# Performance work log

Hardware: AMD Instinct MI355X
Metric: run time of the kernel (lower is better)

The kernel has to match this reference:

```python
import jax, jax.numpy as jnp
import numpy as np

NUM_HEADS = 16
THETA = 10000.0


def setup_inputs() -> dict:
    key = jax.random.key(0)
    k1, k2, k3, k4 = jax.random.split(key, 4)
    B, T, D = 2, 2048, 1024
    x = jax.random.normal(k1, (B, T, D), dtype=jnp.float32)
    token_positions = jnp.sort(
        jax.random.randint(k2, (B, T), 0, 2048), axis=-1
    ).astype(jnp.int32)
    sigma_qkv = float(np.sqrt(2.0 / (D + 3 * D)))
    sigma_out = float(np.sqrt(2.0 / (D + D)))
    W_qkv = jax.random.normal(k3, (3 * D, D), dtype=jnp.float32) * sigma_qkv
    W_out = jax.random.normal(k4, (D, D), dtype=jnp.float32) * sigma_out
    return {"x": x, "token_positions": token_positions, "W_qkv": W_qkv, "W_out": W_out}


def _apply_rope(t, cos, sin):
    # t: [B, H, T, d_k]; cos/sin: [B, T, d_k//2]
    B, H, T, dk = t.shape
    t2 = t.reshape(B, H, T, dk // 2, 2)
    te, to = t2[..., 0], t2[..., 1]
    c = cos[:, None]  # [B, 1, T, dk//2]
    s = sin[:, None]
    ye = te * c - to * s
    yo = to * c + te * s
    return jnp.stack([ye, yo], axis=-1).reshape(B, H, T, dk)


def reference(x, token_positions, W_qkv, W_out):
    B, T, D = x.shape
    H = NUM_HEADS
    dk = D // H

    # fused QKV projection: [B, T, 3D] -> split (three, h, d) on last dim
    qkv = jnp.einsum("btd,od->bto", x, W_qkv).reshape(B, T, 3, H, dk)
    qkv = jnp.transpose(qkv, (2, 0, 3, 1, 4))  # [3, B, H, T, dk]
    q, k, v = qkv[0], qkv[1], qkv[2]

    # RoPE angles from token positions
    n = jnp.arange(dk // 2, dtype=jnp.float32)
    inv_freq = THETA ** (-2.0 * n / dk)  # [dk//2]
    angles = token_positions.astype(jnp.float32)[..., None] * inv_freq  # [B, T, dk//2]
    cos, sin = jnp.cos(angles), jnp.sin(angles)
    q = _apply_rope(q, cos, sin)
    k = _apply_rope(k, cos, sin)

    # causal scaled dot-product attention
    scores = jnp.einsum("bhid,bhjd->bhij", q, k) / jnp.sqrt(jnp.float32(dk))
    causal = jnp.tril(jnp.ones((T, T), dtype=bool))
    scores = jnp.where(causal, scores, -jnp.inf)
    probs = jax.nn.softmax(scores, axis=-1)
    attn = jnp.einsum("bhij,bhjd->bhid", probs, v)  # [B, H, T, dk]

    concat = jnp.transpose(attn, (0, 2, 1, 3)).reshape(B, T, D)
    return jnp.einsum("btd,od->bto", concat, W_out)
```

## Files before the change

### kernel.cpp

```cpp
#include <hip/hip_runtime.h>
#include <hip/hip_bf16.h>
#include <cmath>

#define T_SEQ 2048
#define D_MODEL 1024
#define NHEAD 16
#define DK 64

typedef short bf16x8 __attribute__((ext_vector_type(8)));
typedef float f32x4 __attribute__((ext_vector_type(4)));
typedef float f32x16 __attribute__((ext_vector_type(16)));
typedef unsigned uint2v __attribute__((ext_vector_type(2)));

union U8 { unsigned u[4]; bf16x8 v; };

#define VMCNT(n) asm volatile("s_waitcnt vmcnt(" #n ")" ::: "memory")
#define BAR() __builtin_amdgcn_s_barrier()
#define SFENCE() __builtin_amdgcn_sched_barrier(0)

__device__ __forceinline__ short f2b(float f) {
    unsigned u = __builtin_bit_cast(unsigned, f);
    unsigned r = (u + 0x7FFFu + ((u >> 16) & 1u)) >> 16;
    return (short)r;
}

__device__ __forceinline__ void gll16(const void* g, void* l) {
    __builtin_amdgcn_global_load_lds(
        (__attribute__((address_space(1))) void*)g,
        (__attribute__((address_space(3))) void*)l, 16, 0, 0);
}

__device__ __forceinline__ bf16x8 lds_frag(const short* base, int row, int chunk) {
    return *reinterpret_cast<const bf16x8*>(
        (const char*)base + row * 128 + ((chunk * 16) ^ ((row & 7) << 4)));
}

__device__ __forceinline__ unsigned pkbf16(float a, float b) {
    unsigned r;
    asm("v_cvt_pk_bf16_f32 %0, %1, %2" : "=v"(r) : "v"(a), "v"(b));
    return r;
}
__device__ __forceinline__ void pl32swap(unsigned& a, unsigned& b) {
    uint2v r = __builtin_amdgcn_permlane32_swap(a, b, false, false);
    a = r.x; b = r.y;
}

__global__ __launch_bounds__(256) void cvt_all(const float* __restrict__ x,
                                               const float* __restrict__ wq,
                                               const float* __restrict__ wo,
                                               const int* __restrict__ pos,
                                               short* __restrict__ xb,
                                               short* __restrict__ wqb,
                                               short* __restrict__ wob,
                                               float* __restrict__ ct,
                                               float* __restrict__ st) {
    int i = blockIdx.x * 256 + threadIdx.x;
    if (i >= 1048576) {
        int j = i - 1048576;
        int bt = j >> 5, n = j & 31;
        float p = (float)pos[bt];
        float invf = expf((float)n * (-2.0f / (float)DK) * 9.210340371976184f);
        float s, c;
        sincosf(p * invf, &s, &c);
        ct[j] = c; st[j] = s;
        return;
    }
    const float* src;
    short* dst;
    int srcoff, c;
    if (i < 524288) {
        c = i;
        int tile = c >> 9, cc = c & 511;
        int kblk = cc >> 7, row = cc & 127;
        int rb = tile >> 5, kb = tile & 31;
        srcoff = (rb * 128 + row) * D_MODEL + kb * 32 + kblk * 8;
        src = x; dst = xb;
    } else if (i < 917504) {
        c = i - 524288;
        int tile = c >> 9, cc = c & 511;
        int kblk = cc >> 7, row = cc & 127;
        int rb = tile >> 5, kb = tile & 31;
        srcoff = (rb * 128 + row) * D_MODEL + kb * 32 + kblk * 8;
        src = wq; dst = wqb;
    } else {
        c = i - 917504;
        int tile = c >> 8, cc = c & 255;
        int kblk = cc >> 6, row = cc & 63;
        int nb = tile >> 5, kb = tile & 31;
        srcoff = (nb * 64 + row) * D_MODEL + kb * 32 + kblk * 8;
        src = wo; dst = wob;
    }
    float4 a = *reinterpret_cast<const float4*>(src + srcoff);
    float4 b = *reinterpret_cast<const float4*>(src + srcoff + 4);
    bf16x8 v;
    v[0] = f2b(a.x); v[1] = f2b(a.y); v[2] = f2b(a.z); v[3] = f2b(a.w);
    v[4] = f2b(b.x); v[5] = f2b(b.y); v[6] = f2b(b.z); v[7] = f2b(b.w);
    reinterpret_cast<bf16x8*>(dst)[c] = v;
}

__global__ __launch_bounds__(256, 3) void gemm_qkv(const short* __restrict__ xb,
                                                   const short* __restrict__ wb,
                                                   const float* __restrict__ ct,
                                                   const float* __restrict__ st,
                                                   short* __restrict__ Qo,
                                                   short* __restrict__ Ko,
                                                   short* __restrict__ Vt) {
    __shared__ short SM[3][8192];
    const int tid = threadIdx.x;
    const int w = tid >> 6, l = tid & 63, lg = l >> 4, li = l & 15;
    const int wr = w >> 1, wc = w & 1;
    const int bn = blockIdx.x * 128, bm = blockIdx.y * 128;

    const short* pA = xb + (size_t)blockIdx.y * 32 * 4096 + (w * 128 + l) * 8;
    const short* pB = wb + (size_t)blockIdx.x * 32 * 4096 + (w * 128 + l) * 8;

    f32x4 zero = {0.f, 0.f, 0.f, 0.f};
    f32x4 acc[4][4];
#pragma unroll
    for (int m = 0; m < 4; ++m)
#pragma unroll
        for (int n = 0; n < 4; ++n) acc[m][n] = zero;

#define GSTAGE(buf, t_)                                               \
    do {                                                              \
        const size_t ko = (size_t)(t_) * 4096;                        \
        gll16(pA + ko,       &SM[buf][w * 1024]);                     \
        gll16(pA + ko + 512, &SM[buf][w * 1024 + 512]);               \
        gll16(pB + ko,       &SM[buf][4096 + w * 1024]);              \
        gll16(pB + ko + 512, &SM[buf][4096 + w * 1024 + 512]);        \
    } while (0)

    GSTAGE(0, 0);
    GSTAGE(1, 1);

    for (int t = 0; t < 32; ++t) {
        if (t < 31) { VMCNT(4); } else { VMCNT(0); }
        BAR();
        SFENCE();
        if (t + 2 < 32) GSTAGE((t + 2) % 3, t + 2);
        const short* Ac = &SM[t % 3][0];
        const short* Bc = &SM[t % 3][4096];
        bf16x8 a[4], b[4];
#pragma unroll
        for (int m = 0; m < 4; ++m)
            a[m] = *reinterpret_cast<const bf16x8*>(&Ac[lg * 1024 + (wr * 64 + m * 16 + li) * 8]);
#pragma unroll
        for (int n = 0; n < 4; ++n)
            b[n] = *reinterpret_cast<const bf16x8*>(&Bc[lg * 1024 + (wc * 64 + n * 16 + li) * 8]);
        __builtin_amdgcn_s_setprio(1);
#pragma unroll
        for (int m = 0; m < 4; ++m)
#pragma unroll
            for (int n = 0; n < 4; ++n)
                acc[m][n] = __builtin_amdgcn_mfma_f32_16x16x32_bf16(a[m], b[n], acc[m][n], 0, 0, 0);
        __builtin_amdgcn_s_setprio(0);
    }
#undef GSTAGE

    const int which = bn >> 10;
    const int h = ((bn >> 6) + wc) & 15;
    if (which == 2) {
        __syncthreads();
        short* scr = &SM[0][0] + w * 4096;
#pragma unroll
        for (int n = 0; n < 4; ++n)
#pragma unroll
            for (int m = 0; m < 4; ++m)
#pragma unroll
                for (int rp = 0; rp < 2; ++rp) {
                    int d = n * 16 + li;
                    int t64 = m * 16 + lg * 4 + rp * 2;
                    unsigned pk = pkbf16(acc[m][n][rp * 2], acc[m][n][rp * 2 + 1]);
                    *reinterpret_cast<unsigned*>(
                        (char*)scr + ((d * 128 + t64 * 2) ^ ((d & 7) << 4))) = pk;
                }
        const int mi0 = bm + wr * 64;
        const int b0 = mi0 >> 11, t0 = mi0 & (T_SEQ - 1);
        short* vbase = Vt + (size_t)(b0 * NHEAD + h) * DK * T_SEQ + t0;
#pragma unroll
        for (int db = 0; db < 8; ++db) {
            int d = db * 8 + (l >> 3);
            int ch = l & 7;
            bf16x8 v = *reinterpret_cast<const bf16x8*>(
                (char*)scr + ((d * 128 + ch * 16) ^ ((d & 7) << 4)));
            *reinterpret_cast<bf16x8*>(vbase + (size_t)d * T_SEQ + ch * 8) = v;
        }
    } else {
#pragma unroll
        for (int n = 0; n < 4; ++n) {
            const int d = n * 16 + li;
#pragma unroll
            for (int m = 0; m < 4; ++m)
#pragma unroll
                for (int r = 0; r < 4; ++r) {
                    const int mi = bm + wr * 64 + m * 16 + lg * 4 + r;
                    const int b_ = mi >> 11, tt = mi & (T_SEQ - 1);
                    float v = acc[m][n][r];
                    float vp = __shfl_xor(v, 1);
                    int nn = n * 8 + (li >> 1);
                    float c = ct[(size_t)mi * 32 + nn];
                    float s = st[(size_t)mi * 32 + nn];
                    float o = (d & 1) ? (v * c + vp * s) : (v * c - vp * s);
                    if (which == 0) o *= 0.18033688011112042f;
                    short* dst = (which == 0) ? Qo : Ko;
                    dst[((size_t)((b_ * NHEAD + h) * T_SEQ + tt)) * DK + d] = f2b(o);
                }
        }
    }
}

__global__ __launch_bounds__(256, 2) void attn(const short* __restrict__ Q,
                                               const short* __restrict__ K,
                                               const short* __restrict__ Vt,
                                               short* __restrict__ Cc) {
    __shared__ short Kls[3][4096];
    __shared__ short Vls[3][4096];

    const int bid = blockIdx.x;
    const int ii = bid & 255, rr = bid >> 8;
    const int bh = ii & 31;
    const int qt = rr ? (15 - (ii >> 5)) : (ii >> 5);
    const int blkq0 = qt * 128;
    const int ntb = 2 * qt + 2;

    const int tid = threadIdx.x;
    const int w = tid >> 6, l = tid & 63;
    const int l31 = l & 31, hi = l >> 5, hi4 = hi * 4, hi8 = hi * 8;
    const int q0w = blkq0 + w * 32;

    const short* Qh = Q + (size_t)bh * T_SEQ * DK;
    const short* Kh = K + (size_t)bh * T_SEQ * DK;
    const short* Vh = Vt + (size_t)bh * DK * T_SEQ;

    bf16x8 qf[4];
#pragma unroll
    for (int ks = 0; ks < 4; ++ks)
        qf[ks] = *reinterpret_cast<const bf16x8*>(&Qh[(size_t)(q0w + l31) * DK + ks * 16 + hi8]);

    f32x16 o0 = {0.f,0.f,0.f,0.f,0.f,0.f,0.f,0.f,0.f,0.f,0.f,0.f,0.f,0.f,0.f,0.f};
    f32x16 o1 = o0;
    float m = -3.0e38f;
    float lsum = 0.f;

    const int c0 = w * 128 + l;
    const int c1 = c0 + 64;
    const int r0 = c0 >> 3, cc0 = (c0 & 7) ^ (r0 & 7);
    const int r1 = c1 >> 3, cc1 = (c1 & 7) ^ (r1 & 7);

#define ASTAGE(buf, n0_)                                                                \
    do {                                                                                \
        gll16(Kh + (size_t)((n0_) + r0) * DK + cc0 * 8, &Kls[buf][(2 * w) * 512]);      \
        gll16(Kh + (size_t)((n0_) + r1) * DK + cc1 * 8, &Kls[buf][(2 * w + 1) * 512]);  \
        gll16(Vh + (size_t)r0 * T_SEQ + (n0_) + cc0 * 8, &Vls[buf][(2 * w) * 512]);     \
        gll16(Vh + (size_t)r1 * T_SEQ + (n0_) + cc1 * 8, &Vls[buf][(2 * w + 1) * 512]); \
    } while (0)

    ASTAGE(0, 0);
    ASTAGE(1, 64);

    for (int t = 0; t < ntb; ++t) {
        if (t + 1 < ntb) { VMCNT(4); } else { VMCNT(0); }
        BAR();
        SFENCE();
        if (t + 2 < ntb) ASTAGE((t + 2) % 3, (t + 2) * 64);
        const int n0 = t * 64;

        if (n0 < q0w + 32) {
            const short* Kc = Kls[t % 3];
            const short* Vc = Vls[t % 3];

            f32x16 s0 = {0.f,0.f,0.f,0.f,0.f,0.f,0.f,0.f,0.f,0.f,0.f,0.f,0.f,0.f,0.f,0.f};
            f32x16 s1 = s0;
            __builtin_amdgcn_s_setprio(1);
#pragma unroll
            for (int ks = 0; ks < 4; ++ks) {
                bf16x8 kf0 = lds_frag(Kc, l31,      ks * 2 + hi);
                bf16x8 kf1 = lds_frag(Kc, 32 + l31, ks * 2 + hi);
                s0 = __builtin_amdgcn_mfma_f32_32x32x16_bf16(kf0, qf[ks], s0, 0, 0, 0);
                s1 = __builtin_amdgcn_mfma_f32_32x32x16_bf16(kf1, qf[ks], s1, 0, 0, 0);
            }
            __builtin_amdgcn_s_setprio(0);

            float p[32];
#pragma unroll
            for (int r = 0; r < 16; ++r) { p[r] = s0[r]; p[16 + r] = s1[r]; }

            if (n0 + 64 > q0w) {
                const int qrel = q0w + l31 - n0;
#pragma unroll
                for (int r = 0; r < 16; ++r) {
                    const int kvm = (r & 3) + 8 * (r >> 2) + hi4;
                    if (kvm > qrel) p[r] = -3.0e38f;
                    if (kvm + 32 > qrel) p[16 + r] = -3.0e38f;
                }
            }

            float t16[16];
#pragma unroll
            for (int r = 0; r < 16; ++r) t16[r] = fmaxf(p[r], p[16 + r]);
#pragma unroll
            for (int d = 8; d >= 1; d >>= 1)
#pragma unroll
                for (int r = 0; r < 8; ++r)
                    if (r < d) t16[r] = fmaxf(t16[r], t16[r + d]);
            float tmax = fmaxf(t16[0], __shfl_xor(t16[0], 32));

            if (__any(tmax > m + 8.0f)) {
                float mnew = fmaxf(m, tmax);
                float alpha = __builtin_amdgcn_exp2f(m - mnew);
                m = mnew;
#pragma unroll
                for (int r = 0; r < 16; ++r) {
                    float ar = __shfl(alpha, (r & 3) + 8 * (r >> 2) + hi4);
                    o0[r] *= ar; o1[r] *= ar;
                }
                lsum *= alpha;
            }

#pragma unroll
            for (int r = 0; r < 32; ++r) p[r] = __builtin_amdgcn_exp2f(p[r] - m);
            float a16[16];
#pragma unroll
            for (int r = 0; r < 16; ++r) a16[r] = p[r] + p[16 + r];
#pragma unroll
            for (int d = 8; d >= 1; d >>= 1)
#pragma unroll
                for (int r = 0; r < 8; ++r)
                    if (r < d) a16[r] += a16[r + d];
            lsum += a16[0] + __shfl_xor(a16[0], 32);

            __builtin_amdgcn_s_setprio(1);
#pragma unroll
            for (int kb = 0; kb < 2; ++kb) {
                unsigned pk0 = pkbf16(p[kb * 16 + 0],  p[kb * 16 + 1]);
                unsigned pk1 = pkbf16(p[kb * 16 + 2],  p[kb * 16 + 3]);
                unsigned pk2 = pkbf16(p[kb * 16 + 4],  p[kb * 16 + 5]);
                unsigned pk3 = pkbf16(p[kb * 16 + 6],  p[kb * 16 + 7]);
                unsigned pk4 = pkbf16(p[kb * 16 + 8],  p[kb * 16 + 9]);
                unsigned pk5 = pkbf16(p[kb * 16 + 10], p[kb * 16 + 11]);
                unsigned pk6 = pkbf16(p[kb * 16 + 12], p[kb * 16 + 13]);
                unsigned pk7 = pkbf16(p[kb * 16 + 14], p[kb * 16 + 15]);
                pl32swap(pk0, pk2); pl32swap(pk1, pk3);
                pl32swap(pk4, pk6); pl32swap(pk5, pk7);
                U8 f0, f1;
                f0.u[0] = pk0; f0.u[1] = pk1; f0.u[2] = pk2; f0.u[3] = pk3;
                f1.u[0] = pk4; f1.u[1] = pk5; f1.u[2] = pk6; f1.u[3] = pk7;
                bf16x8 v00 = lds_frag(Vc, l31,      kb * 4 + hi);
                bf16x8 v01 = lds_frag(Vc, l31,      kb * 4 + 2 + hi);
                bf16x8 v10 = lds_frag(Vc, 32 + l31, kb * 4 + hi);
                bf16x8 v11 = lds_frag(Vc, 32 + l31, kb * 4 + 2 + hi);
                o0 = __builtin_amdgcn_mfma_f32_32x32x16_bf16(f0.v, v00, o0, 0, 0, 0);
                o0 = __builtin_amdgcn_mfma_f32_32x32x16_bf16(f1.v, v01, o0, 0, 0, 0);
                o1 = __builtin_amdgcn_mfma_f32_32x32x16_bf16(f0.v, v10, o1, 0, 0, 0);
                o1 = __builtin_amdgcn_mfma_f32_32x32x16_bf16(f1.v, v11, o1, 0, 0, 0);
            }
            __builtin_amdgcn_s_setprio(0);
        }
    }
#undef ASTAGE

    const int b = bh >> 4, h = bh & 15;
    const float linv = 1.0f / lsum;
#pragma unroll
    for (int r = 0; r < 16; ++r) {
        const int qoff = (r & 3) + 8 * (r >> 2) + hi4;
        float inv = __shfl(linv, qoff);
        const int mg = b * T_SEQ + q0w + qoff;
        const int mb = mg >> 7, row = mg & 127;
        const int kblk = (l31 >> 3) & 3, el = l & 7;
        Cc[((size_t)(mb * 32 + h * 2 + 0)) * 4096 + kblk * 1024 + row * 8 + el] = f2b(o0[r] * inv);
        Cc[((size_t)(mb * 32 + h * 2 + 1)) * 4096 + kblk * 1024 + row * 8 + el] = f2b(o1[r] * inv);
    }
}

__global__ __launch_bounds__(256, 3) void gemm_out(const short* __restrict__ ab,
                                                   const short* __restrict__ wb,
                                                   float* __restrict__ out) {
    __shared__ short SM[3][6144];
    const int tid = threadIdx.x;
    const int w = tid >> 6, l = tid & 63, lg = l >> 4, li = l & 15;
    const int wr = w >> 1, wc = w & 1;
    const int bn = blockIdx.x * 64, bm = blockIdx.y * 128;

    const short* pA = ab + (size_t)blockIdx.y * 32 * 4096 + (w * 128 + l) * 8;
    const short* pB = wb + (size_t)blockIdx.x * 32 * 2048 + (w * 64 + l) * 8;

    f32x4 zero = {0.f, 0.f, 0.f, 0.f};
    f32x4 acc[4][2];
#pragma unroll
    for (int m = 0; m < 4; ++m)
#pragma unroll
        for (int n = 0; n < 2; ++n) acc[m][n] = zero;

#define OSTAGE(buf, t_)                                                  \
    do {                                                                 \
        gll16(pA + (size_t)(t_) * 4096,       &SM[buf][w * 1024]);       \
        gll16(pA + (size_t)(t_) * 4096 + 512, &SM[buf][w * 1024 + 512]); \
        gll16(pB + (size_t)(t_) * 2048,       &SM[buf][4096 + w * 512]); \
    } while (0)

    OSTAGE(0, 0);
    OSTAGE(1, 1);

    for (int t = 0; t < 32; ++t) {
        if (t < 31) { VMCNT(3); } else { VMCNT(0); }
        BAR();
        SFENCE();
        if (t + 2 < 32) OSTAGE((t + 2) % 3, t + 2);
        const short* Ac = &SM[t % 3][0];
        const short* Bc = &SM[t % 3][4096];
        bf16x8 a[4], b[2];
#pragma unroll
        for (int m = 0; m < 4; ++m)
            a[m] = *reinterpret_cast<const bf16x8*>(&Ac[lg * 1024 + (wr * 64 + m * 16 + li) * 8]);
#pragma unroll
        for (int n = 0; n < 2; ++n)
            b[n] = *reinterpret_cast<const bf16x8*>(&Bc[lg * 512 + (wc * 32 + n * 16 + li) * 8]);
        __builtin_amdgcn_s_setprio(1);
#pragma unroll
        for (int m = 0; m < 4; ++m)
#pragma unroll
            for (int n = 0; n < 2; ++n)
                acc[m][n] = __builtin_amdgcn_mfma_f32_16x16x32_bf16(a[m], b[n], acc[m][n], 0, 0, 0);
        __builtin_amdgcn_s_setprio(0);
    }
#undef OSTAGE

#pragma unroll
    for (int m = 0; m < 4; ++m)
#pragma unroll
        for (int n = 0; n < 2; ++n)
#pragma unroll
            for (int r = 0; r < 4; ++r) {
                const int mi = bm + wr * 64 + m * 16 + lg * 4 + r;
                out[(size_t)mi * D_MODEL + bn + wc * 32 + n * 16 + li] = acc[m][n][r];
            }
}

extern "C" void kernel_launch(void* const* d_in, const int* in_sizes, int n_in,
                              void* d_out, int out_size, void* d_ws, size_t ws_size,
                              hipStream_t stream) {
    const float* x    = (const float*)d_in[0];
    const int*   pos  = (const int*)d_in[1];
    const float* wqkv = (const float*)d_in[2];
    const float* wout = (const float*)d_in[3];
    float* out = (float*)d_out;

    char* ws = (char*)d_ws;
    size_t off = 0;
    short* xb  = (short*)(ws + off); off += (size_t)4096 * 1024 * 2;
    short* wqb = (short*)(ws + off); off += (size_t)3072 * 1024 * 2;
    short* wob = (short*)(ws + off); off += (size_t)1024 * 1024 * 2;
    short* Q   = (short*)(ws + off); off += (size_t)32 * 2048 * 64 * 2;
    short* Kb  = (short*)(ws + off); off += (size_t)32 * 2048 * 64 * 2;
    short* Vt  = (short*)(ws + off); off += (size_t)32 * 64 * 2048 * 2;
    off += 4096;
    short* Cc  = (short*)(ws + off); off += (size_t)4096 * 1024 * 2;
    float* ct  = (float*)(ws + off); off += (size_t)4096 * 32 * 4;
    float* st  = (float*)(ws + off); off += (size_t)4096 * 32 * 4;

    cvt_all<<<4608, 256, 0, stream>>>(x, wqkv, wout, pos, xb, wqb, wob, ct, st);
    gemm_qkv<<<dim3(24, 32), 256, 0, stream>>>(xb, wqb, ct, st, Q, Kb, Vt);
    attn<<<512, 256, 0, stream>>>(Q, Kb, Vt, Cc);
    gemm_out<<<dim3(16, 32), 256, 0, stream>>>(Cc, wob, out);
}
```

Before: 114.3 us.

## Split attention KV range across wave pairs and merge partial softmax states

The attention kernel now uses 64-query tiles, doubling the grid to 1024 blocks. Within a block, two wave pairs each handle the same 32 queries but alternate KV tiles, and their partial outputs, maxima and sums are merged through shared memory at the end. LDS staging drops from triple to double buffering with a full vmcnt wait, which allows more blocks per CU. This targets better load balance and occupancy on the causal workload, at the cost of less load/compute overlap, an extra merge step, and each wave computing only half the tiles it waits on.

```diff
diff --git a/kernel.cpp b/kernel.cpp
--- a/kernel.cpp
+++ b/kernel.cpp
@@ -209,24 +209,26 @@
     }
 }
 
-__global__ __launch_bounds__(256, 2) void attn(const short* __restrict__ Q,
+__global__ __launch_bounds__(256, 4) void attn(const short* __restrict__ Q,
                                                const short* __restrict__ K,
                                                const short* __restrict__ Vt,
                                                short* __restrict__ Cc) {
-    __shared__ short Kls[3][4096];
-    __shared__ short Vls[3][4096];
+    __shared__ short Kls[2][4096];
+    __shared__ short Vls[2][4096];
+    __shared__ float MLp[2][2][32];
 
     const int bid = blockIdx.x;
-    const int ii = bid & 255, rr = bid >> 8;
+    const int half = bid >> 9;
+    const int ii = bid & 511;
     const int bh = ii & 31;
-    const int qt = rr ? (15 - (ii >> 5)) : (ii >> 5);
-    const int blkq0 = qt * 128;
-    const int ntb = 2 * qt + 2;
+    const int qt = half ? (31 - (ii >> 5)) : (ii >> 5);
+    const int ntb = qt + 1;
 
     const int tid = threadIdx.x;
     const int w = tid >> 6, l = tid & 63;
     const int l31 = l & 31, hi = l >> 5, hi4 = hi * 4, hi8 = hi * 8;
-    const int q0w = blkq0 + w * 32;
+    const int qpar = w & 1, tpar = w >> 1;
+    const int q0w = qt * 64 + qpar * 32;
 
     const short* Qh = Q + (size_t)bh * T_SEQ * DK;
     const short* Kh = K + (size_t)bh * T_SEQ * DK;
@@ -256,18 +258,17 @@
     } while (0)
 
     ASTAGE(0, 0);
-    ASTAGE(1, 64);
 
     for (int t = 0; t < ntb; ++t) {
-        if (t + 1 < ntb) { VMCNT(4); } else { VMCNT(0); }
+        VMCNT(0);
         BAR();
         SFENCE();
-        if (t + 2 < ntb) ASTAGE((t + 2) % 3, (t + 2) * 64);
+        if (t + 1 < ntb) ASTAGE((t + 1) & 1, (t + 1) * 64);
         const int n0 = t * 64;
 
-        if (n0 < q0w + 32) {
-            const short* Kc = Kls[t % 3];
-            const short* Vc = Vls[t % 3];
+        if (((t ^ tpar) & 1) == 0) {
+            const short* Kc = Kls[t & 1];
+            const short* Vc = Vls[t & 1];
 
             f32x16 s0 = {0.f,0.f,0.f,0.f,0.f,0.f,0.f,0.f,0.f,0.f,0.f,0.f,0.f,0.f,0.f,0.f};
             f32x16 s1 = s0;
@@ -359,17 +360,46 @@
     }
 #undef ASTAGE
 
-    const int b = bh >> 4, h = bh & 15;
-    const float linv = 1.0f / lsum;
-#pragma unroll
-    for (int r = 0; r < 16; ++r) {
-        const int qoff = (r & 3) + 8 * (r >> 2) + hi4;
-        float inv = __shfl(linv, qoff);
-        const int mg = b * T_SEQ + q0w + qoff;
-        const int mb = mg >> 7, row = mg & 127;
-        const int kblk = (l31 >> 3) & 3, el = l & 7;
-        Cc[((size_t)(mb * 32 + h * 2 + 0)) * 4096 + kblk * 1024 + row * 8 + el] = f2b(o0[r] * inv);
-        Cc[((size_t)(mb * 32 + h * 2 + 1)) * 4096 + kblk * 1024 + row * 8 + el] = f2b(o1[r] * inv);
+    __syncthreads();
+    float* Opool = reinterpret_cast<float*>(&Kls[0][0]);
+    const int vq = hi * 256 + l31;
+    if (w >= 2) {
+        float* Ow = Opool + (w - 2) * 2048;
+#pragma unroll
+        for (int r = 0; r < 16; ++r) {
+            const int qbase = ((r & 3) + 8 * (r >> 2)) * 64;
+            Ow[qbase + vq] = o0[r];
+            Ow[qbase + vq + 32] = o1[r];
+        }
+        if (l < 32) { MLp[w - 2][0][l] = m; MLp[w - 2][1][l] = lsum; }
+    }
+    __syncthreads();
+    if (w < 2) {
+        const float m2 = MLp[w][0][l31];
+        const float l2 = MLp[w][1][l31];
+        const float M = fmaxf(m, m2);
+        const float a1 = __builtin_amdgcn_exp2f(m - M);
+        const float a2 = __builtin_amdgcn_exp2f(m2 - M);
+        const float linv = 1.0f / (lsum * a1 + l2 * a2);
+        const float* Ow = Opool + w * 2048;
+        const int b = bh >> 4, h = bh & 15;
+#pragma unroll
+        for (int r = 0; r < 16; ++r) {
+            const int qoff = (r & 3) + 8 * (r >> 2) + hi4;
+            const float a1r = __shfl(a1, qoff);
+            const float a2r = __shfl(a2, qoff);
+            const float ir  = __shfl(linv, qoff);
+            const int qbase = ((r & 3) + 8 * (r >> 2)) * 64;
+            const float p0 = Ow[qbase + vq];
+            const float p1 = Ow[qbase + vq + 32];
+            const float f0 = (o0[r] * a1r + p0 * a2r) * ir;
+            const float f1 = (o1[r] * a1r + p1 * a2r) * ir;
+            const int mg = b * T_SEQ + q0w + qoff;
+            const int mb = mg >> 7, row = mg & 127;
+            const int kblk = (l31 >> 3) & 3, el = l & 7;
+            Cc[((size_t)(mb * 32 + h * 2 + 0)) * 4096 + kblk * 1024 + row * 8 + el] = f2b(f0);
+            Cc[((size_t)(mb * 32 + h * 2 + 1)) * 4096 + kblk * 1024 + row * 8 + el] = f2b(f1);
+        }
     }
 }
 
@@ -461,6 +491,6 @@
 
     cvt_all<<<4608, 256, 0, stream>>>(x, wqkv, wout, pos, xb, wqb, wob, ct, st);
     gemm_qkv<<<dim3(24, 32), 256, 0, stream>>>(xb, wqb, ct, st, Q, Kb, Vt);
-    attn<<<512, 256, 0, stream>>>(Q, Kb, Vt, Cc);
+    attn<<<1024, 256, 0, stream>>>(Q, Kb, Vt, Cc);
     gemm_out<<<dim3(16, 32), 256, 0, stream>>>(Cc, wob, out);
 }
```

Result: slower. 120.8 us (+5.7%).

## Split attention into 64-row query blocks with two waves and double buffering

Applied to the files above, without the earlier changes.

The attention kernel now launches 1024 blocks of 128 threads, each covering 64 query rows, instead of 512 blocks of 256 threads covering 128 rows with paired causal tiles. The launch order runs the longest query tiles first, and the per-wave skip of fully masked KV tiles is gone because each block's KV range now matches its rows exactly. The K/V LDS pipeline drops from a triple buffer to a double buffer, and each iteration waits for all loads before computing. The aim is finer-grained causal load balancing and less LDS per block for higher occupancy, at the cost of reloading K/V once per 64 rows instead of once per 128 and less overlap between memory loads and compute.

```diff
diff --git a/kernel.cpp b/kernel.cpp
--- a/kernel.cpp
+++ b/kernel.cpp
@@ -209,24 +209,22 @@
     }
 }
 
-__global__ __launch_bounds__(256, 2) void attn(const short* __restrict__ Q,
+__global__ __launch_bounds__(128, 2) void attn(const short* __restrict__ Q,
                                                const short* __restrict__ K,
                                                const short* __restrict__ Vt,
                                                short* __restrict__ Cc) {
-    __shared__ short Kls[3][4096];
-    __shared__ short Vls[3][4096];
+    __shared__ short Kls[2][4096];
+    __shared__ short Vls[2][4096];
 
     const int bid = blockIdx.x;
-    const int ii = bid & 255, rr = bid >> 8;
-    const int bh = ii & 31;
-    const int qt = rr ? (15 - (ii >> 5)) : (ii >> 5);
-    const int blkq0 = qt * 128;
-    const int ntb = 2 * qt + 2;
+    const int bh = bid & 31;
+    const int qt = 31 - (bid >> 5);
+    const int ntb = qt + 1;
 
     const int tid = threadIdx.x;
     const int w = tid >> 6, l = tid & 63;
     const int l31 = l & 31, hi = l >> 5, hi4 = hi * 4, hi8 = hi * 8;
-    const int q0w = blkq0 + w * 32;
+    const int q0w = qt * 64 + w * 32;
 
     const short* Qh = Q + (size_t)bh * T_SEQ * DK;
     const short* Kh = K + (size_t)bh * T_SEQ * DK;
@@ -242,122 +240,121 @@
     float m = -3.0e38f;
     float lsum = 0.f;
 
-    const int c0 = w * 128 + l;
-    const int c1 = c0 + 64;
-    const int r0 = c0 >> 3, cc0 = (c0 & 7) ^ (r0 & 7);
-    const int r1 = c1 >> 3, cc1 = (c1 & 7) ^ (r1 & 7);
-
-#define ASTAGE(buf, n0_)                                                                \
-    do {                                                                                \
-        gll16(Kh + (size_t)((n0_) + r0) * DK + cc0 * 8, &Kls[buf][(2 * w) * 512]);      \
-        gll16(Kh + (size_t)((n0_) + r1) * DK + cc1 * 8, &Kls[buf][(2 * w + 1) * 512]);  \
-        gll16(Vh + (size_t)r0 * T_SEQ + (n0_) + cc0 * 8, &Vls[buf][(2 * w) * 512]);     \
-        gll16(Vh + (size_t)r1 * T_SEQ + (n0_) + cc1 * 8, &Vls[buf][(2 * w + 1) * 512]); \
-    } while (0)
-
-    ASTAGE(0, 0);
-    ASTAGE(1, 64);
+    int rr[4], cb[4];
+#pragma unroll
+    for (int j = 0; j < 4; ++j) {
+        int c = j * 128 + tid;
+        rr[j] = c >> 3;
+        cb[j] = ((c & 7) ^ (rr[j] & 7)) * 8;
+    }
+
+    auto astage = [&](int buf, int n0_) {
+#pragma unroll
+        for (int j = 0; j < 4; ++j)
+            gll16(Kh + (size_t)(n0_ + rr[j]) * DK + cb[j], &Kls[buf][j * 1024 + w * 512]);
+#pragma unroll
+        for (int j = 0; j < 4; ++j)
+            gll16(Vh + (size_t)rr[j] * T_SEQ + n0_ + cb[j], &Vls[buf][j * 1024 + w * 512]);
+    };
+
+    astage(0, 0);
 
     for (int t = 0; t < ntb; ++t) {
-        if (t + 1 < ntb) { VMCNT(4); } else { VMCNT(0); }
+        VMCNT(0);
         BAR();
         SFENCE();
-        if (t + 2 < ntb) ASTAGE((t + 2) % 3, (t + 2) * 64);
+        if (t + 1 < ntb) astage((t + 1) & 1, (t + 1) * 64);
         const int n0 = t * 64;
-
-        if (n0 < q0w + 32) {
-            const short* Kc = Kls[t % 3];
-            const short* Vc = Vls[t % 3];
-
-            f32x16 s0 = {0.f,0.f,0.f,0.f,0.f,0.f,0.f,0.f,0.f,0.f,0.f,0.f,0.f,0.f,0.f,0.f};
-            f32x16 s1 = s0;
-            __builtin_amdgcn_s_setprio(1);
-#pragma unroll
-            for (int ks = 0; ks < 4; ++ks) {
-                bf16x8 kf0 = lds_frag(Kc, l31,      ks * 2 + hi);
-                bf16x8 kf1 = lds_frag(Kc, 32 + l31, ks * 2 + hi);
-                s0 = __builtin_amdgcn_mfma_f32_32x32x16_bf16(kf0, qf[ks], s0, 0, 0, 0);
-                s1 = __builtin_amdgcn_mfma_f32_32x32x16_bf16(kf1, qf[ks], s1, 0, 0, 0);
+        const short* Kc = Kls[t & 1];
+        const short* Vc = Vls[t & 1];
+
+        f32x16 s0 = {0.f,0.f,0.f,0.f,0.f,0.f,0.f,0.f,0.f,0.f,0.f,0.f,0.f,0.f,0.f,0.f};
+        f32x16 s1 = s0;
+        __builtin_amdgcn_s_setprio(1);
+#pragma unroll
+        for (int ks = 0; ks < 4; ++ks) {
+            bf16x8 kf0 = lds_frag(Kc, l31,      ks * 2 + hi);
+            bf16x8 kf1 = lds_frag(Kc, 32 + l31, ks * 2 + hi);
+            s0 = __builtin_amdgcn_mfma_f32_32x32x16_bf16(kf0, qf[ks], s0, 0, 0, 0);
+            s1 = __builtin_amdgcn_mfma_f32_32x32x16_bf16(kf1, qf[ks], s1, 0, 0, 0);
+        }
+        __builtin_amdgcn_s_setprio(0);
+
+        float p[32];
+#pragma unroll
+        for (int r = 0; r < 16; ++r) { p[r] = s0[r]; p[16 + r] = s1[r]; }
+
+        if (n0 + 64 > q0w) {
+            const int qrel = q0w + l31 - n0;
+#pragma unroll
+            for (int r = 0; r < 16; ++r) {
+                const int kvm = (r & 3) + 8 * (r >> 2) + hi4;
+                if (kvm > qrel) p[r] = -3.0e38f;
+                if (kvm + 32 > qrel) p[16 + r] = -3.0e38f;
             }
-            __builtin_amdgcn_s_setprio(0);
-
-            float p[32];
-#pragma unroll
-            for (int r = 0; r < 16; ++r) { p[r] = s0[r]; p[16 + r] = s1[r]; }
-
-            if (n0 + 64 > q0w) {
-                const int qrel = q0w + l31 - n0;
-#pragma unroll
-                for (int r = 0; r < 16; ++r) {
-                    const int kvm = (r & 3) + 8 * (r >> 2) + hi4;
-                    if (kvm > qrel) p[r] = -3.0e38f;
-                    if (kvm + 32 > qrel) p[16 + r] = -3.0e38f;
-                }
+        }
+
+        float t16[16];
+#pragma unroll
+        for (int r = 0; r < 16; ++r) t16[r] = fmaxf(p[r], p[16 + r]);
+#pragma unroll
+        for (int d = 8; d >= 1; d >>= 1)
+#pragma unroll
+            for (int r = 0; r < 8; ++r)
+                if (r < d) t16[r] = fmaxf(t16[r], t16[r + d]);
+        float tmax = fmaxf(t16[0], __shfl_xor(t16[0], 32));
+
+        if (__any(tmax > m + 8.0f)) {
+            float mnew = fmaxf(m, tmax);
+            float alpha = __builtin_amdgcn_exp2f(m - mnew);
+            m = mnew;
+#pragma unroll
+            for (int r = 0; r < 16; ++r) {
+                float ar = __shfl(alpha, (r & 3) + 8 * (r >> 2) + hi4);
+                o0[r] *= ar; o1[r] *= ar;
             }
-
-            float t16[16];
-#pragma unroll
-            for (int r = 0; r < 16; ++r) t16[r] = fmaxf(p[r], p[16 + r]);
-#pragma unroll
-            for (int d = 8; d >= 1; d >>= 1)
-#pragma unroll
-                for (int r = 0; r < 8; ++r)
-                    if (r < d) t16[r] = fmaxf(t16[r], t16[r + d]);
-            float tmax = fmaxf(t16[0], __shfl_xor(t16[0], 32));
-
-            if (__any(tmax > m + 8.0f)) {
-                float mnew = fmaxf(m, tmax);
-                float alpha = __builtin_amdgcn_exp2f(m - mnew);
-                m = mnew;
-#pragma unroll
-                for (int r = 0; r < 16; ++r) {
-                    float ar = __shfl(alpha, (r & 3) + 8 * (r >> 2) + hi4);
-                    o0[r] *= ar; o1[r] *= ar;
-                }
-                lsum *= alpha;
-            }
-
-#pragma unroll
-            for (int r = 0; r < 32; ++r) p[r] = __builtin_amdgcn_exp2f(p[r] - m);
-            float a16[16];
-#pragma unroll
-            for (int r = 0; r < 16; ++r) a16[r] = p[r] + p[16 + r];
-#pragma unroll
-            for (int d = 8; d >= 1; d >>= 1)
-#pragma unroll
-                for (int r = 0; r < 8; ++r)
-                    if (r < d) a16[r] += a16[r + d];
-            lsum += a16[0] + __shfl_xor(a16[0], 32);
-
-            __builtin_amdgcn_s_setprio(1);
-#pragma unroll
-            for (int kb = 0; kb < 2; ++kb) {
-                unsigned pk0 = pkbf16(p[kb * 16 + 0],  p[kb * 16 + 1]);
-                unsigned pk1 = pkbf16(p[kb * 16 + 2],  p[kb * 16 + 3]);
-                unsigned pk2 = pkbf16(p[kb * 16 + 4],  p[kb * 16 + 5]);
-                unsigned pk3 = pkbf16(p[kb * 16 + 6],  p[kb * 16 + 7]);
-                unsigned pk4 = pkbf16(p[kb * 16 + 8],  p[kb * 16 + 9]);
-                unsigned pk5 = pkbf16(p[kb * 16 + 10], p[kb * 16 + 11]);
-                unsigned pk6 = pkbf16(p[kb * 16 + 12], p[kb * 16 + 13]);
-                unsigned pk7 = pkbf16(p[kb * 16 + 14], p[kb * 16 + 15]);
-                pl32swap(pk0, pk2); pl32swap(pk1, pk3);
-                pl32swap(pk4, pk6); pl32swap(pk5, pk7);
-                U8 f0, f1;
-                f0.u[0] = pk0; f0.u[1] = pk1; f0.u[2] = pk2; f0.u[3] = pk3;
-                f1.u[0] = pk4; f1.u[1] = pk5; f1.u[2] = pk6; f1.u[3] = pk7;
-                bf16x8 v00 = lds_frag(Vc, l31,      kb * 4 + hi);
-                bf16x8 v01 = lds_frag(Vc, l31,      kb * 4 + 2 + hi);
-                bf16x8 v10 = lds_frag(Vc, 32 + l31, kb * 4 + hi);
-                bf16x8 v11 = lds_frag(Vc, 32 + l31, kb * 4 + 2 + hi);
-                o0 = __builtin_amdgcn_mfma_f32_32x32x16_bf16(f0.v, v00, o0, 0, 0, 0);
-                o0 = __builtin_amdgcn_mfma_f32_32x32x16_bf16(f1.v, v01, o0, 0, 0, 0);
-                o1 = __builtin_amdgcn_mfma_f32_32x32x16_bf16(f0.v, v10, o1, 0, 0, 0);
-                o1 = __builtin_amdgcn_mfma_f32_32x32x16_bf16(f1.v, v11, o1, 0, 0, 0);
-            }
-            __builtin_amdgcn_s_setprio(0);
-        }
-    }
-#undef ASTAGE
+            lsum *= alpha;
+        }
+
+#pragma unroll
+        for (int r = 0; r < 32; ++r) p[r] = __builtin_amdgcn_exp2f(p[r] - m);
+        float a16[16];
+#pragma unroll
+        for (int r = 0; r < 16; ++r) a16[r] = p[r] + p[16 + r];
+#pragma unroll
+        for (int d = 8; d >= 1; d >>= 1)
+#pragma unroll
+            for (int r = 0; r < 8; ++r)
+                if (r < d) a16[r] += a16[r + d];
+        lsum += a16[0] + __shfl_xor(a16[0], 32);
+
+        __builtin_amdgcn_s_setprio(1);
+#pragma unroll
+        for (int kb = 0; kb < 2; ++kb) {
+            unsigned pk0 = pkbf16(p[kb * 16 + 0],  p[kb * 16 + 1]);
+            unsigned pk1 = pkbf16(p[kb * 16 + 2],  p[kb * 16 + 3]);
+            unsigned pk2 = pkbf16(p[kb * 16 + 4],  p[kb * 16 + 5]);
+            unsigned pk3 = pkbf16(p[kb * 16 + 6],  p[kb * 16 + 7]);
+            unsigned pk4 = pkbf16(p[kb * 16 + 8],  p[kb * 16 + 9]);
+            unsigned pk5 = pkbf16(p[kb * 16 + 10], p[kb * 16 + 11]);
+            unsigned pk6 = pkbf16(p[kb * 16 + 12], p[kb * 16 + 13]);
+            unsigned pk7 = pkbf16(p[kb * 16 + 14], p[kb * 16 + 15]);
+            pl32swap(pk0, pk2); pl32swap(pk1, pk3);
+            pl32swap(pk4, pk6); pl32swap(pk5, pk7);
+            U8 f0, f1;
+            f0.u[0] = pk0; f0.u[1] = pk1; f0.u[2] = pk2; f0.u[3] = pk3;
+            f1.u[0] = pk4; f1.u[1] = pk5; f1.u[2] = pk6; f1.u[3] = pk7;
+            bf16x8 v00 = lds_frag(Vc, l31,      kb * 4 + hi);
+            bf16x8 v01 = lds_frag(Vc, l31,      kb * 4 + 2 + hi);
+            bf16x8 v10 = lds_frag(Vc, 32 + l31, kb * 4 + hi);
+            bf16x8 v11 = lds_frag(Vc, 32 + l31, kb * 4 + 2 + hi);
+            o0 = __builtin_amdgcn_mfma_f32_32x32x16_bf16(f0.v, v00, o0, 0, 0, 0);
+            o0 = __builtin_amdgcn_mfma_f32_32x32x16_bf16(f1.v, v01, o0, 0, 0, 0);
+            o1 = __builtin_amdgcn_mfma_f32_32x32x16_bf16(f0.v, v10, o1, 0, 0, 0);
+            o1 = __builtin_amdgcn_mfma_f32_32x32x16_bf16(f1.v, v11, o1, 0, 0, 0);
+        }
+        __builtin_amdgcn_s_setprio(0);
+    }
 
     const int b = bh >> 4, h = bh & 15;
     const float linv = 1.0f / lsum;
@@ -367,7 +364,7 @@
         float inv = __shfl(linv, qoff);
         const int mg = b * T_SEQ + q0w + qoff;
         const int mb = mg >> 7, row = mg & 127;
-        const int kblk = (l31 >> 3) & 3, el = l & 7;
+        const int kblk = l31 >> 3, el = l & 7;
         Cc[((size_t)(mb * 32 + h * 2 + 0)) * 4096 + kblk * 1024 + row * 8 + el] = f2b(o0[r] * inv);
         Cc[((size_t)(mb * 32 + h * 2 + 1)) * 4096 + kblk * 1024 + row * 8 + el] = f2b(o1[r] * inv);
     }
@@ -461,6 +458,6 @@
 
     cvt_all<<<4608, 256, 0, stream>>>(x, wqkv, wout, pos, xb, wqb, wob, ct, st);
     gemm_qkv<<<dim3(24, 32), 256, 0, stream>>>(xb, wqb, ct, st, Q, Kb, Vt);
-    attn<<<512, 256, 0, stream>>>(Q, Kb, Vt, Cc);
+    attn<<<1024, 128, 0, stream>>>(Q, Kb, Vt, Cc);
     gemm_out<<<dim3(16, 32), 256, 0, stream>>>(Cc, wob, out);
 }
```

After: 115.2 us. No clear change (+0.8%).
